# Performance work log

Measured on AMD Instinct MI355X. Metric: run time of the kernel, lower is better.

## Reference

```python
import jax, jax.numpy as jnp
import numpy as np

INPUT_SIZE = 512
OUTPUT_CLASS = 2
BATCH, INST_NUM = 4, 40000


def setup_inputs() -> dict:
    key = jax.random.key(0)
    ks = jax.random.split(key, 8)
    s_in = 1.0 / np.sqrt(INPUT_SIZE)
    s_h = 1.0 / np.sqrt(128)
    return {
        "feats": jax.random.normal(ks[0], (BATCH, INST_NUM, INPUT_SIZE), jnp.float32),
        "c": jax.random.normal(ks[1], (BATCH, INST_NUM, OUTPUT_CLASS), jnp.float32),
        "q_w1": jax.random.uniform(ks[2], (INPUT_SIZE, 128), jnp.float32, -s_in, s_in),
        "q_b1": jax.random.uniform(ks[3], (128,), jnp.float32, -s_in, s_in),
        "q_w2": jax.random.uniform(ks[4], (128, 128), jnp.float32, -s_h, s_h),
        "q_b2": jax.random.uniform(ks[5], (128,), jnp.float32, -s_h, s_h),
        "fcc_w": jax.random.uniform(ks[6], (OUTPUT_CLASS, OUTPUT_CLASS, INPUT_SIZE), jnp.float32, -s_in, s_in),
        "fcc_b": jax.random.uniform(ks[7], (OUTPUT_CLASS,), jnp.float32, -s_in, s_in),
    }


def _q_mlp(x, w1, b1, w2, b2):
    h = jax.nn.relu(x @ w1 + b1)
    return jnp.tanh(h @ w2 + b2)


def reference(feats, c, q_w1, q_b1, q_w2, q_b2, fcc_w, fcc_b):
    batch, inst_num, dim = feats.shape
    V = feats  # passing_v=False -> Identity
    Q = _q_mlp(feats, q_w1, q_b1, q_w2, q_b2)  # [b, n, 128]
    # top instance per class: sort descending, take first -> argmax along instances
    top_idx = jnp.argmax(c, axis=1)  # [b, output_class]
    m_feats = jnp.take_along_axis(feats, top_idx[:, :, None], axis=1)  # [b, oc, dim]
    q_max = _q_mlp(m_feats, q_w1, q_b1, q_w2, q_b2)  # [b, oc, 128]
    # NOTE: original divides by sqrt(Q.shape[1]) == sqrt(inst_num)
    scale = jnp.sqrt(jnp.float32(inst_num))
    A = jnp.einsum('bnk,bok->bno', Q, q_max) / scale  # [b, n, oc]
    A = jax.nn.softmax(A, axis=1)  # softmax over instances
    B = jnp.einsum('bno,bnd->bod', A, V)  # [b, oc, dim]
    # Conv1d(oc, oc, kernel=dim) on B -> full contraction over (in_ch, dim)
    C = jnp.einsum('bid,oid->bo', B, fcc_w) + fcc_b  # [b, oc]
    return C, A, B
```

## Files before the change

### kernel.cpp

```cpp
#include <hip/hip_runtime.h>
#include <hip/hip_bf16.h>

#define NB 4
#define NI 40000
#define DI 512
#define NH 128
#define TM 32
#define NT 1250

typedef __attribute__((ext_vector_type(8))) short bf16x8;
typedef __attribute__((ext_vector_type(4))) float f32x4;

__device__ __forceinline__ ushort f2b(float f) {
    union { float f; unsigned u; } x; x.f = f;
    unsigned r = x.u + 0x7FFFu + ((x.u >> 16) & 1u);
    return (ushort)(r >> 16);
}
__device__ __forceinline__ float b2f(ushort u) {
    union { unsigned u; float f; } x; x.u = ((unsigned)u) << 16;
    return x.f;
}

__global__ void k_wt(const float* __restrict__ w1, const float* __restrict__ w2,
                     ushort* __restrict__ w1t, ushort* __restrict__ w2t) {
    int idx = blockIdx.x * 256 + threadIdx.x;
    if (idx < 65536) {
        int j = idx >> 9, i = idx & 511;
        w1t[idx] = f2b(w1[i * 128 + j]);
    } else if (idx < 81920) {
        int r = idx - 65536;
        int j = r >> 7, k = r & 127;
        w2t[r] = f2b(w2[k * 128 + j]);
    }
}

__global__ void k_am1(const float* __restrict__ c, float* __restrict__ pv, int* __restrict__ pi) {
    int blk = blockIdx.x;
    int bo = blk >> 4, ch = blk & 15;
    int b = bo >> 1, o = bo & 1;
    __shared__ float rv[256];
    __shared__ int   ri[256];
    int tid = threadIdx.x;
    float bv = -3.402823466e38f; int bi = 0x7fffffff;
    for (int n = ch * 2500 + tid; n < (ch + 1) * 2500; n += 256) {
        float v = c[((size_t)b * NI + n) * 2 + o];
        if (v > bv || (v == bv && n < bi)) { bv = v; bi = n; }
    }
    rv[tid] = bv; ri[tid] = bi;
    __syncthreads();
    for (int s = 128; s > 0; s >>= 1) {
        if (tid < s) {
            if (rv[tid + s] > rv[tid] || (rv[tid + s] == rv[tid] && ri[tid + s] < ri[tid])) {
                rv[tid] = rv[tid + s]; ri[tid] = ri[tid + s];
            }
        }
        __syncthreads();
    }
    if (tid == 0) { pv[blk] = rv[0]; pi[blk] = ri[0]; }
}

__global__ void k_am2(const float* __restrict__ pv, const int* __restrict__ pi,
                      int* __restrict__ topidx) {
    int bo = blockIdx.x;
    if (threadIdx.x == 0) {
        float bv = -3.402823466e38f; int bi = 0x7fffffff;
        for (int ch = 0; ch < 16; ++ch) {
            float v = pv[bo * 16 + ch]; int idx = pi[bo * 16 + ch];
            if (v > bv || (v == bv && idx < bi)) { bv = v; bi = idx; }
        }
        topidx[bo] = bi;
    }
}

__global__ void k_qmax(const float* __restrict__ feats, const int* __restrict__ topidx,
                       const float* __restrict__ w1, const float* __restrict__ b1,
                       const float* __restrict__ w2, const float* __restrict__ b2,
                       float* __restrict__ qmax) {
    int bo = blockIdx.x;
    int b = bo >> 1;
    __shared__ float xs[DI];
    __shared__ float hs[NH];
    int tid = threadIdx.x;
    const float* x = feats + ((size_t)b * NI + topidx[bo]) * DI;
    if (tid < DI) xs[tid] = x[tid];
    __syncthreads();
    int j = tid >> 2, part = tid & 3;
    float p = 0.f;
    for (int i = part * 128; i < part * 128 + 128; ++i)
        p += xs[i] * w1[i * NH + j];
    p += __shfl_xor(p, 1); p += __shfl_xor(p, 2);
    if (part == 0) { float h = p + b1[j]; hs[j] = h > 0.f ? h : 0.f; }
    __syncthreads();
    p = 0.f;
    for (int i = part * 32; i < part * 32 + 32; ++i)
        p += hs[i] * w2[i * NH + j];
    p += __shfl_xor(p, 1); p += __shfl_xor(p, 2);
    if (part == 0) qmax[bo * NH + j] = tanhf(p + b2[j]);
}

__global__ __launch_bounds__(256, 3)
void k_main(const float* __restrict__ feats,
            const ushort* __restrict__ w1t, const ushort* __restrict__ w2t,
            const float* __restrict__ b1, const float* __restrict__ b2,
            const float* __restrict__ qmax,
            float* __restrict__ s_ws, float* __restrict__ zp, float* __restrict__ Up) {
    __shared__ ushort x_lds[TM * 512];
    __shared__ ushort h_lds[TM * 128];
    __shared__ float  sp_lds[4][TM][2];
    __shared__ float  e_lds[TM * 2];
    __shared__ float  qm_lds[2 * NH];

    const int tid = threadIdx.x;
    const int b = blockIdx.x / NT;
    const int t = blockIdx.x % NT;
    const int n0 = t * TM;

    qm_lds[tid] = qmax[b * 256 + tid];

    const float4* xg4 = (const float4*)(feats + ((size_t)(b * NI + n0)) * DI);
#pragma unroll
    for (int q = 0; q < 16; ++q) {
        int idx = tid + q * 256;
        int row = idx >> 7;
        int c4  = idx & 127;
        float4 v = xg4[idx];
        ushort4 u;
        u.x = f2b(v.x); u.y = f2b(v.y); u.z = f2b(v.z); u.w = f2b(v.w);
        int byteoff = (c4 * 8) ^ ((row & 7) << 4);
        *(ushort4*)((char*)x_lds + row * 1024 + byteoff) = u;
    }
    __syncthreads();

    const int wn = tid >> 6;
    const int lane = tid & 63;
    const int lr = lane & 15;
    const int lk = (lane >> 4) * 8;
    const int l4 = (lane >> 4) * 4;
    const int xsw = (lr & 7) << 4;

    const char* xrow0 = (const char*)x_lds + lr * 1024;
    const char* xrow1 = (const char*)x_lds + (16 + lr) * 1024;
    const ushort* w1b0 = w1t + (size_t)(wn * 32 + lr) * DI + lk;
    const ushort* w1b1 = w1t + (size_t)(wn * 32 + 16 + lr) * DI + lk;

    f32x4 acc[2][2] = {};
#pragma unroll 4
    for (int ks = 0; ks < 16; ++ks) {
        int kb = (ks * 32 + lk) * 2;
        bf16x8 a0 = *(const bf16x8*)(xrow0 + (kb ^ xsw));
        bf16x8 a1 = *(const bf16x8*)(xrow1 + (kb ^ xsw));
        bf16x8 b0 = *(const bf16x8*)(w1b0 + ks * 32);
        bf16x8 b1v = *(const bf16x8*)(w1b1 + ks * 32);
        acc[0][0] = __builtin_amdgcn_mfma_f32_16x16x32_bf16(a0, b0,  acc[0][0], 0, 0, 0);
        acc[0][1] = __builtin_amdgcn_mfma_f32_16x16x32_bf16(a0, b1v, acc[0][1], 0, 0, 0);
        acc[1][0] = __builtin_amdgcn_mfma_f32_16x16x32_bf16(a1, b0,  acc[1][0], 0, 0, 0);
        acc[1][1] = __builtin_amdgcn_mfma_f32_16x16x32_bf16(a1, b1v, acc[1][1], 0, 0, 0);
    }

#pragma unroll
    for (int m = 0; m < 2; ++m)
#pragma unroll
        for (int n = 0; n < 2; ++n) {
            int col = wn * 32 + n * 16 + lr;
            float bias = b1[col];
#pragma unroll
            for (int r = 0; r < 4; ++r) {
                int row = m * 16 + l4 + r;
                float v = acc[m][n][r] + bias;
                *(ushort*)((char*)h_lds + row * 256 + ((col * 2) ^ ((row & 7) << 4))) =
                    f2b(v > 0.f ? v : 0.f);
            }
        }
    __syncthreads();

    f32x4 acc2[2][2] = {};
#pragma unroll
    for (int ks = 0; ks < 4; ++ks) {
        int kb = (ks * 32 + lk) * 2;
        bf16x8 a0 = *(const bf16x8*)((const char*)h_lds + lr * 256 + (kb ^ xsw));
        bf16x8 a1 = *(const bf16x8*)((const char*)h_lds + (16 + lr) * 256 + (kb ^ xsw));
        bf16x8 b0 = *(const bf16x8*)(w2t + (wn * 32 + lr) * NH + ks * 32 + lk);
        bf16x8 b1v = *(const bf16x8*)(w2t + (wn * 32 + 16 + lr) * NH + ks * 32 + lk);
        acc2[0][0] = __builtin_amdgcn_mfma_f32_16x16x32_bf16(a0, b0,  acc2[0][0], 0, 0, 0);
        acc2[0][1] = __builtin_amdgcn_mfma_f32_16x16x32_bf16(a0, b1v, acc2[0][1], 0, 0, 0);
        acc2[1][0] = __builtin_amdgcn_mfma_f32_16x16x32_bf16(a1, b0,  acc2[1][0], 0, 0, 0);
        acc2[1][1] = __builtin_amdgcn_mfma_f32_16x16x32_bf16(a1, b1v, acc2[1][1], 0, 0, 0);
    }

#pragma unroll
    for (int m = 0; m < 2; ++m)
#pragma unroll
        for (int r = 0; r < 4; ++r) {
            float p0 = 0.f, p1 = 0.f;
#pragma unroll
            for (int n = 0; n < 2; ++n) {
                int col = wn * 32 + n * 16 + lr;
                float q = tanhf(acc2[m][n][r] + b2[col]);
                p0 += q * qm_lds[col];
                p1 += q * qm_lds[NH + col];
            }
            p0 += __shfl_xor(p0, 1); p1 += __shfl_xor(p1, 1);
            p0 += __shfl_xor(p0, 2); p1 += __shfl_xor(p1, 2);
            p0 += __shfl_xor(p0, 4); p1 += __shfl_xor(p1, 4);
            p0 += __shfl_xor(p0, 8); p1 += __shfl_xor(p1, 8);
            if (lr == 0) {
                int row = m * 16 + l4 + r;
                sp_lds[wn][row][0] = p0;
                sp_lds[wn][row][1] = p1;
            }
        }
    __syncthreads();

    if (tid < 64) {
        int row = tid >> 1, o = tid & 1;
        float s = (sp_lds[0][row][o] + sp_lds[1][row][o] +
                   sp_lds[2][row][o] + sp_lds[3][row][o]) * 0.005f;
        s_ws[((size_t)(b * NI + n0 + row)) * 2 + o] = s;
        float e = expf(s);
        e_lds[row * 2 + o] = e;
        float z = e;
        z += __shfl_xor(z, 2);  z += __shfl_xor(z, 4);
        z += __shfl_xor(z, 8);  z += __shfl_xor(z, 16);
        z += __shfl_xor(z, 32);
        if (tid < 2) zp[(b * NT + t) * 2 + tid] = z;
    }
    __syncthreads();

    {
        int bc = tid * 4;
        float u00 = 0.f, u01 = 0.f, u10 = 0.f, u11 = 0.f;
#pragma unroll 8
        for (int n = 0; n < TM; ++n) {
            unsigned v = *(const unsigned*)((const char*)x_lds + n * 1024 + (bc ^ ((n & 7) << 4)));
            float x0 = b2f((ushort)(v & 0xffff));
            float x1 = b2f((ushort)(v >> 16));
            float e0 = e_lds[n * 2], e1 = e_lds[n * 2 + 1];
            u00 += e0 * x0; u01 += e0 * x1;
            u10 += e1 * x0; u11 += e1 * x1;
        }
        size_t base = ((size_t)(b * NT + t) * 2) * DI;
        float2 v0; v0.x = u00; v0.y = u01;
        float2 v1; v1.x = u10; v1.y = u11;
        *(float2*)&Up[base + tid * 2] = v0;
        *(float2*)&Up[base + DI + tid * 2] = v1;
    }
}

__global__ void k_zred(const float* __restrict__ zp, float* __restrict__ Zt) {
    int bo = blockIdx.x; int b = bo >> 1, o = bo & 1;
    __shared__ float red[256];
    int tid = threadIdx.x;
    float z = 0.f;
    for (int t = tid; t < NT; t += 256) z += zp[(b * NT + t) * 2 + o];
    red[tid] = z; __syncthreads();
    for (int s = 128; s > 0; s >>= 1) {
        if (tid < s) red[tid] += red[tid + s];
        __syncthreads();
    }
    if (tid == 0) Zt[bo] = red[0];
}

__global__ void k_A(const float* __restrict__ s_ws, const float* __restrict__ Zt,
                    float* __restrict__ outA) {
    int idx = blockIdx.x * 256 + threadIdx.x;
    int b = idx / (NI * 2);
    int o = idx & 1;
    outA[idx] = expf(s_ws[idx]) / Zt[b * 2 + o];
}

__global__ void k_B1(const float* __restrict__ Up, float* __restrict__ Up2) {
    int blk = blockIdx.x;
    int bo = blk / 25, cch = blk % 25;
    int b = bo >> 1, o = bo & 1;
    int d = threadIdx.x;
    float u = 0.f;
    for (int t = cch * 50; t < cch * 50 + 50; ++t)
        u += Up[(((size_t)(b * NT + t)) * 2 + o) * DI + d];
    Up2[(size_t)blk * DI + d] = u;
}

__global__ void k_B2(const float* __restrict__ Up2, const float* __restrict__ Zt,
                     float* __restrict__ outB) {
    int bo = blockIdx.x; int d = threadIdx.x;
    float u = 0.f;
    for (int cc = 0; cc < 25; ++cc) u += Up2[(size_t)(bo * 25 + cc) * DI + d];
    outB[bo * DI + d] = u / Zt[bo];
}

__global__ void k_C(const float* __restrict__ outB, const float* __restrict__ fcc_w,
                    const float* __restrict__ fcc_b, float* __restrict__ outC) {
    int bo = blockIdx.x; int b = bo >> 1, o = bo & 1;
    __shared__ float red[256];
    int tid = threadIdx.x;
    float acc = 0.f;
    for (int idx = tid; idx < 2 * DI; idx += 256) {
        int i = idx >> 9, d = idx & 511;
        acc += outB[(b * 2 + i) * DI + d] * fcc_w[o * (2 * DI) + i * DI + d];
    }
    red[tid] = acc; __syncthreads();
    for (int s = 128; s > 0; s >>= 1) {
        if (tid < s) red[tid] += red[tid + s];
        __syncthreads();
    }
    if (tid == 0) outC[bo] = red[0] + fcc_b[o];
}

extern "C" void kernel_launch(void* const* d_in, const int* in_sizes, int n_in,
                              void* d_out, int out_size, void* d_ws, size_t ws_size,
                              hipStream_t stream) {
    const float* feats = (const float*)d_in[0];
    const float* c     = (const float*)d_in[1];
    const float* q_w1  = (const float*)d_in[2];
    const float* q_b1  = (const float*)d_in[3];
    const float* q_w2  = (const float*)d_in[4];
    const float* q_b2  = (const float*)d_in[5];
    const float* fcc_w = (const float*)d_in[6];
    const float* fcc_b = (const float*)d_in[7];
    float* out = (float*)d_out;

    char* w = (char*)d_ws;
    ushort* w1t  = (ushort*)(w);
    ushort* w2t  = (ushort*)(w + 131072);
    float* qmaxb = (float*)(w + 163840);
    int*   topi  = (int*)(w + 167936);
    float* Zt    = (float*)(w + 167968);
    float* pv    = (float*)(w + 168000);
    int*   pi    = (int*)(w + 168512);
    float* s_ws  = (float*)(w + 169024);
    float* zp    = (float*)(w + 1449024);
    float* Up2   = (float*)(w + 1489024);
    float* Up    = (float*)(w + 1898624);

    float* outC = out;
    float* outA = out + 8;
    float* outB = out + 8 + NB * NI * 2;

    k_wt<<<320, 256, 0, stream>>>(q_w1, q_w2, w1t, w2t);
    k_am1<<<128, 256, 0, stream>>>(c, pv, pi);
    k_am2<<<8, 64, 0, stream>>>(pv, pi, topi);
    k_qmax<<<8, 512, 0, stream>>>(feats, topi, q_w1, q_b1, q_w2, q_b2, qmaxb);
    k_main<<<NB * NT, 256, 0, stream>>>(feats, w1t, w2t, q_b1, q_b2, qmaxb, s_ws, zp, Up);
    k_zred<<<8, 256, 0, stream>>>(zp, Zt);
    k_A<<<NB * NI * 2 / 256, 256, 0, stream>>>(s_ws, Zt, outA);
    k_B1<<<200, 512, 0, stream>>>(Up, Up2);
    k_B2<<<8, 512, 0, stream>>>(Up2, Zt, outB);
    k_C<<<8, 256, 0, stream>>>(outB, fcc_w, fcc_b, outC);
}
```

Baseline: 204.4 us.

## Make main kernel persistent with double-buffered feature prefetch and register-resident weights

The main kernel becomes persistent: 128 blocks per batch loop over tiles with a stride, prefetching the next tile's features into registers and writing them into a second LDS buffer while the current tile is computed. W2 fragments, biases and qmax values are held in registers, W1 fragments are software-prefetched in groups, and tanh/exp use fast approximations. Per-block partial sums shrink, so the two-stage B reduction collapses into one kernel and the Z reduction uses a single wave. The changes add LDS and register pressure (occupancy bound lowered to 2) and slightly reduce numerical accuracy from the fast tanh/exp.

```diff
diff --git a/kernel.cpp b/kernel.cpp
--- a/kernel.cpp
+++ b/kernel.cpp
@@ -7,6 +7,7 @@
 #define NH 128
 #define TM 32
 #define NT 1250
+#define SUBB 128
 
 typedef __attribute__((ext_vector_type(8))) short bf16x8;
 typedef __attribute__((ext_vector_type(4))) float f32x4;
@@ -19,6 +20,11 @@
 __device__ __forceinline__ float b2f(ushort u) {
     union { unsigned u; float f; } x; x.u = ((unsigned)u) << 16;
     return x.f;
+}
+__device__ __forceinline__ float tanh_fast(float x) {
+    x = fminf(15.f, fmaxf(-15.f, x));
+    float e = __expf(2.f * x);
+    return (e - 1.f) / (e + 1.f);
 }
 
 __global__ void k_wt(const float* __restrict__ w1, const float* __restrict__ w2,
@@ -98,38 +104,51 @@
     if (part == 0) qmax[bo * NH + j] = tanhf(p + b2[j]);
 }
 
-__global__ __launch_bounds__(256, 3)
+#define L1G(C0, C1, N0, N1, G)                                                  \
+  {                                                                             \
+    if ((G) < 3) {                                                              \
+      _Pragma("unroll")                                                         \
+      for (int j = 0; j < 4; ++j) {                                             \
+        N0[j] = *(const bf16x8*)(wb0 + ((G) + 1) * 128 + j * 32);               \
+        N1[j] = *(const bf16x8*)(wb1 + ((G) + 1) * 128 + j * 32);               \
+      }                                                                         \
+    }                                                                           \
+    _Pragma("unroll")                                                           \
+    for (int j = 0; j < 4; ++j) {                                               \
+      int kb = (((G) * 4 + j) * 32 + lk) * 2;                                   \
+      bf16x8 a0 = *(const bf16x8*)(xrow0 + (kb ^ xsw));                         \
+      bf16x8 a1 = *(const bf16x8*)(xrow1 + (kb ^ xsw));                         \
+      acc00 = __builtin_amdgcn_mfma_f32_16x16x32_bf16(a0, C0[j], acc00, 0, 0, 0);\
+      acc01 = __builtin_amdgcn_mfma_f32_16x16x32_bf16(a0, C1[j], acc01, 0, 0, 0);\
+      acc10 = __builtin_amdgcn_mfma_f32_16x16x32_bf16(a1, C0[j], acc10, 0, 0, 0);\
+      acc11 = __builtin_amdgcn_mfma_f32_16x16x32_bf16(a1, C1[j], acc11, 0, 0, 0);\
+    }                                                                           \
+  }
+
+#define EPI1(ACC, M, N, BIAS)                                                   \
+  _Pragma("unroll")                                                             \
+  for (int r = 0; r < 4; ++r) {                                                 \
+    int row = (M) * 16 + l4 + r;                                                \
+    float v = ACC[r] + (BIAS);                                                  \
+    *(ushort*)((char*)h_lds + row * 256 +                                       \
+               (((wn * 32 + (N) * 16 + lr) * 2) ^ ((row & 7) << 4))) =          \
+        f2b(v > 0.f ? v : 0.f);                                                 \
+  }
+
+__global__ __launch_bounds__(256, 2)
 void k_main(const float* __restrict__ feats,
             const ushort* __restrict__ w1t, const ushort* __restrict__ w2t,
             const float* __restrict__ b1, const float* __restrict__ b2,
             const float* __restrict__ qmax,
             float* __restrict__ s_ws, float* __restrict__ zp, float* __restrict__ Up) {
-    __shared__ ushort x_lds[TM * 512];
+    __shared__ ushort x_lds[2 * TM * 512];
     __shared__ ushort h_lds[TM * 128];
     __shared__ float  sp_lds[4][TM][2];
     __shared__ float  e_lds[TM * 2];
-    __shared__ float  qm_lds[2 * NH];
 
     const int tid = threadIdx.x;
-    const int b = blockIdx.x / NT;
-    const int t = blockIdx.x % NT;
-    const int n0 = t * TM;
-
-    qm_lds[tid] = qmax[b * 256 + tid];
-
-    const float4* xg4 = (const float4*)(feats + ((size_t)(b * NI + n0)) * DI);
-#pragma unroll
-    for (int q = 0; q < 16; ++q) {
-        int idx = tid + q * 256;
-        int row = idx >> 7;
-        int c4  = idx & 127;
-        float4 v = xg4[idx];
-        ushort4 u;
-        u.x = f2b(v.x); u.y = f2b(v.y); u.z = f2b(v.z); u.w = f2b(v.w);
-        int byteoff = (c4 * 8) ^ ((row & 7) << 4);
-        *(ushort4*)((char*)x_lds + row * 1024 + byteoff) = u;
-    }
-    __syncthreads();
+    const int sub = blockIdx.x & (SUBB - 1);
+    const int b   = blockIdx.x >> 7;
 
     const int wn = tid >> 6;
     const int lane = tid & 63;
@@ -138,126 +157,174 @@
     const int l4 = (lane >> 4) * 4;
     const int xsw = (lr & 7) << 4;
 
-    const char* xrow0 = (const char*)x_lds + lr * 1024;
-    const char* xrow1 = (const char*)x_lds + (16 + lr) * 1024;
-    const ushort* w1b0 = w1t + (size_t)(wn * 32 + lr) * DI + lk;
-    const ushort* w1b1 = w1t + (size_t)(wn * 32 + 16 + lr) * DI + lk;
-
-    f32x4 acc[2][2] = {};
-#pragma unroll 4
-    for (int ks = 0; ks < 16; ++ks) {
-        int kb = (ks * 32 + lk) * 2;
-        bf16x8 a0 = *(const bf16x8*)(xrow0 + (kb ^ xsw));
-        bf16x8 a1 = *(const bf16x8*)(xrow1 + (kb ^ xsw));
-        bf16x8 b0 = *(const bf16x8*)(w1b0 + ks * 32);
-        bf16x8 b1v = *(const bf16x8*)(w1b1 + ks * 32);
-        acc[0][0] = __builtin_amdgcn_mfma_f32_16x16x32_bf16(a0, b0,  acc[0][0], 0, 0, 0);
-        acc[0][1] = __builtin_amdgcn_mfma_f32_16x16x32_bf16(a0, b1v, acc[0][1], 0, 0, 0);
-        acc[1][0] = __builtin_amdgcn_mfma_f32_16x16x32_bf16(a1, b0,  acc[1][0], 0, 0, 0);
-        acc[1][1] = __builtin_amdgcn_mfma_f32_16x16x32_bf16(a1, b1v, acc[1][1], 0, 0, 0);
-    }
-
-#pragma unroll
-    for (int m = 0; m < 2; ++m)
-#pragma unroll
-        for (int n = 0; n < 2; ++n) {
-            int col = wn * 32 + n * 16 + lr;
-            float bias = b1[col];
+    const int col0 = wn * 32 + lr;
+    const int col1 = col0 + 16;
+    const float rb1_0 = b1[col0], rb1_1 = b1[col1];
+    const float rb2_0 = b2[col0], rb2_1 = b2[col1];
+    const float qm00 = qmax[b * 256 + col0];
+    const float qm01 = qmax[b * 256 + col1];
+    const float qm10 = qmax[b * 256 + NH + col0];
+    const float qm11 = qmax[b * 256 + NH + col1];
+
+    bf16x8 W2f0[4], W2f1[4];
+#pragma unroll
+    for (int ks = 0; ks < 4; ++ks) {
+        W2f0[ks] = *(const bf16x8*)&w2t[(size_t)col0 * NH + ks * 32 + lk];
+        W2f1[ks] = *(const bf16x8*)&w2t[(size_t)col1 * NH + ks * 32 + lk];
+    }
+
+    const ushort* wb0 = w1t + (size_t)(wn * 32 + lr) * DI + lk;
+    const ushort* wb1 = wb0 + (size_t)16 * DI;
+
+    float u00 = 0.f, u01 = 0.f, u10 = 0.f, u11 = 0.f;
+    float zacc = 0.f;
+
+    float4 pf[16];
+
+    {
+        const float4* xg4 = (const float4*)(feats + ((size_t)b * NI + sub * TM) * DI);
+#pragma unroll
+        for (int q = 0; q < 16; ++q) pf[q] = xg4[tid + q * 256];
+#pragma unroll
+        for (int q = 0; q < 16; ++q) {
+            int idx = tid + q * 256;
+            int row = idx >> 7, c4 = idx & 127;
+            unsigned lo, hi;
+            asm("v_cvt_pk_bf16_f32 %0, %1, %2" : "=v"(lo) : "v"(pf[q].x), "v"(pf[q].y));
+            asm("v_cvt_pk_bf16_f32 %0, %1, %2" : "=v"(hi) : "v"(pf[q].z), "v"(pf[q].w));
+            uint2 u; u.x = lo; u.y = hi;
+            *(uint2*)((char*)x_lds + row * 1024 + ((c4 * 8) ^ ((row & 7) << 4))) = u;
+        }
+    }
+    __syncthreads();
+
+    int cur = 0;
+    for (int t = sub; t < NT; t += SUBB) {
+        const int nxt = cur ^ 1;
+        const bool more = (t + SUBB < NT);
+
+        if (more) {
+            const float4* xg4 = (const float4*)(feats + ((size_t)b * NI + (t + SUBB) * TM) * DI);
+#pragma unroll
+            for (int q = 0; q < 16; ++q) pf[q] = xg4[tid + q * 256];
+        }
+
+        const char* xrow0 = (const char*)x_lds + cur * 32768 + lr * 1024;
+        const char* xrow1 = (const char*)x_lds + cur * 32768 + (16 + lr) * 1024;
+
+        f32x4 acc00 = {}, acc01 = {}, acc10 = {}, acc11 = {};
+        bf16x8 BA0[4], BA1[4], BB0[4], BB1[4];
+#pragma unroll
+        for (int j = 0; j < 4; ++j) {
+            BA0[j] = *(const bf16x8*)(wb0 + j * 32);
+            BA1[j] = *(const bf16x8*)(wb1 + j * 32);
+        }
+        L1G(BA0, BA1, BB0, BB1, 0)
+        L1G(BB0, BB1, BA0, BA1, 1)
+        L1G(BA0, BA1, BB0, BB1, 2)
+        L1G(BB0, BB1, BA0, BA1, 3)
+
+        EPI1(acc00, 0, 0, rb1_0)
+        EPI1(acc01, 0, 1, rb1_1)
+        EPI1(acc10, 1, 0, rb1_0)
+        EPI1(acc11, 1, 1, rb1_1)
+        __syncthreads();
+
+        f32x4 c200 = {}, c201 = {}, c210 = {}, c211 = {};
+#pragma unroll
+        for (int ks = 0; ks < 4; ++ks) {
+            int kb = (ks * 32 + lk) * 2;
+            bf16x8 a0 = *(const bf16x8*)((const char*)h_lds + lr * 256 + (kb ^ xsw));
+            bf16x8 a1 = *(const bf16x8*)((const char*)h_lds + (16 + lr) * 256 + (kb ^ xsw));
+            c200 = __builtin_amdgcn_mfma_f32_16x16x32_bf16(a0, W2f0[ks], c200, 0, 0, 0);
+            c201 = __builtin_amdgcn_mfma_f32_16x16x32_bf16(a0, W2f1[ks], c201, 0, 0, 0);
+            c210 = __builtin_amdgcn_mfma_f32_16x16x32_bf16(a1, W2f0[ks], c210, 0, 0, 0);
+            c211 = __builtin_amdgcn_mfma_f32_16x16x32_bf16(a1, W2f1[ks], c211, 0, 0, 0);
+        }
+
+#pragma unroll
+        for (int m = 0; m < 2; ++m)
 #pragma unroll
             for (int r = 0; r < 4; ++r) {
-                int row = m * 16 + l4 + r;
-                float v = acc[m][n][r] + bias;
-                *(ushort*)((char*)h_lds + row * 256 + ((col * 2) ^ ((row & 7) << 4))) =
-                    f2b(v > 0.f ? v : 0.f);
+                float q0 = tanh_fast((m ? c210[r] : c200[r]) + rb2_0);
+                float q1 = tanh_fast((m ? c211[r] : c201[r]) + rb2_1);
+                float p0 = q0 * qm00 + q1 * qm01;
+                float p1 = q0 * qm10 + q1 * qm11;
+                p0 += __shfl_xor(p0, 1); p1 += __shfl_xor(p1, 1);
+                p0 += __shfl_xor(p0, 2); p1 += __shfl_xor(p1, 2);
+                p0 += __shfl_xor(p0, 4); p1 += __shfl_xor(p1, 4);
+                p0 += __shfl_xor(p0, 8); p1 += __shfl_xor(p1, 8);
+                if (lr == 0) {
+                    int row = m * 16 + l4 + r;
+                    sp_lds[wn][row][0] = p0;
+                    sp_lds[wn][row][1] = p1;
+                }
             }
-        }
-    __syncthreads();
-
-    f32x4 acc2[2][2] = {};
-#pragma unroll
-    for (int ks = 0; ks < 4; ++ks) {
-        int kb = (ks * 32 + lk) * 2;
-        bf16x8 a0 = *(const bf16x8*)((const char*)h_lds + lr * 256 + (kb ^ xsw));
-        bf16x8 a1 = *(const bf16x8*)((const char*)h_lds + (16 + lr) * 256 + (kb ^ xsw));
-        bf16x8 b0 = *(const bf16x8*)(w2t + (wn * 32 + lr) * NH + ks * 32 + lk);
-        bf16x8 b1v = *(const bf16x8*)(w2t + (wn * 32 + 16 + lr) * NH + ks * 32 + lk);
-        acc2[0][0] = __builtin_amdgcn_mfma_f32_16x16x32_bf16(a0, b0,  acc2[0][0], 0, 0, 0);
-        acc2[0][1] = __builtin_amdgcn_mfma_f32_16x16x32_bf16(a0, b1v, acc2[0][1], 0, 0, 0);
-        acc2[1][0] = __builtin_amdgcn_mfma_f32_16x16x32_bf16(a1, b0,  acc2[1][0], 0, 0, 0);
-        acc2[1][1] = __builtin_amdgcn_mfma_f32_16x16x32_bf16(a1, b1v, acc2[1][1], 0, 0, 0);
-    }
-
-#pragma unroll
-    for (int m = 0; m < 2; ++m)
-#pragma unroll
-        for (int r = 0; r < 4; ++r) {
-            float p0 = 0.f, p1 = 0.f;
-#pragma unroll
-            for (int n = 0; n < 2; ++n) {
-                int col = wn * 32 + n * 16 + lr;
-                float q = tanhf(acc2[m][n][r] + b2[col]);
-                p0 += q * qm_lds[col];
-                p1 += q * qm_lds[NH + col];
+        __syncthreads();
+
+        if (tid < 64) {
+            int row = tid >> 1, o = tid & 1;
+            float s = (sp_lds[0][row][o] + sp_lds[1][row][o] +
+                       sp_lds[2][row][o] + sp_lds[3][row][o]) * 0.005f;
+            s_ws[((size_t)(b * NI + t * TM + row)) * 2 + o] = s;
+            float e = __expf(s);
+            e_lds[row * 2 + o] = e;
+            float z = e;
+            z += __shfl_xor(z, 2);  z += __shfl_xor(z, 4);
+            z += __shfl_xor(z, 8);  z += __shfl_xor(z, 16);
+            z += __shfl_xor(z, 32);
+            if (tid < 2) zacc += z;
+        }
+
+        if (more) {
+#pragma unroll
+            for (int q = 0; q < 16; ++q) {
+                int idx = tid + q * 256;
+                int row = idx >> 7, c4 = idx & 127;
+                unsigned lo, hi;
+                asm("v_cvt_pk_bf16_f32 %0, %1, %2" : "=v"(lo) : "v"(pf[q].x), "v"(pf[q].y));
+                asm("v_cvt_pk_bf16_f32 %0, %1, %2" : "=v"(hi) : "v"(pf[q].z), "v"(pf[q].w));
+                uint2 u; u.x = lo; u.y = hi;
+                *(uint2*)((char*)x_lds + nxt * 32768 + row * 1024 + ((c4 * 8) ^ ((row & 7) << 4))) = u;
             }
-            p0 += __shfl_xor(p0, 1); p1 += __shfl_xor(p1, 1);
-            p0 += __shfl_xor(p0, 2); p1 += __shfl_xor(p1, 2);
-            p0 += __shfl_xor(p0, 4); p1 += __shfl_xor(p1, 4);
-            p0 += __shfl_xor(p0, 8); p1 += __shfl_xor(p1, 8);
-            if (lr == 0) {
-                int row = m * 16 + l4 + r;
-                sp_lds[wn][row][0] = p0;
-                sp_lds[wn][row][1] = p1;
+        }
+        __syncthreads();
+
+        {
+            int bc = tid * 4;
+#pragma unroll 8
+            for (int n = 0; n < TM; ++n) {
+                unsigned v = *(const unsigned*)((const char*)x_lds + cur * 32768 +
+                                                n * 1024 + (bc ^ ((n & 7) << 4)));
+                float x0 = b2f((ushort)(v & 0xffff));
+                float x1 = b2f((ushort)(v >> 16));
+                float e0 = e_lds[n * 2], e1 = e_lds[n * 2 + 1];
+                u00 += e0 * x0; u01 += e0 * x1;
+                u10 += e1 * x0; u11 += e1 * x1;
             }
         }
-    __syncthreads();
-
-    if (tid < 64) {
-        int row = tid >> 1, o = tid & 1;
-        float s = (sp_lds[0][row][o] + sp_lds[1][row][o] +
-                   sp_lds[2][row][o] + sp_lds[3][row][o]) * 0.005f;
-        s_ws[((size_t)(b * NI + n0 + row)) * 2 + o] = s;
-        float e = expf(s);
-        e_lds[row * 2 + o] = e;
-        float z = e;
-        z += __shfl_xor(z, 2);  z += __shfl_xor(z, 4);
-        z += __shfl_xor(z, 8);  z += __shfl_xor(z, 16);
-        z += __shfl_xor(z, 32);
-        if (tid < 2) zp[(b * NT + t) * 2 + tid] = z;
-    }
-    __syncthreads();
+        __syncthreads();
+        cur = nxt;
+    }
 
     {
-        int bc = tid * 4;
-        float u00 = 0.f, u01 = 0.f, u10 = 0.f, u11 = 0.f;
-#pragma unroll 8
-        for (int n = 0; n < TM; ++n) {
-            unsigned v = *(const unsigned*)((const char*)x_lds + n * 1024 + (bc ^ ((n & 7) << 4)));
-            float x0 = b2f((ushort)(v & 0xffff));
-            float x1 = b2f((ushort)(v >> 16));
-            float e0 = e_lds[n * 2], e1 = e_lds[n * 2 + 1];
-            u00 += e0 * x0; u01 += e0 * x1;
-            u10 += e1 * x0; u11 += e1 * x1;
-        }
-        size_t base = ((size_t)(b * NT + t) * 2) * DI;
+        size_t base = ((size_t)(b * SUBB + sub) * 2) * DI;
         float2 v0; v0.x = u00; v0.y = u01;
         float2 v1; v1.x = u10; v1.y = u11;
         *(float2*)&Up[base + tid * 2] = v0;
         *(float2*)&Up[base + DI + tid * 2] = v1;
+        if (tid < 2) zp[(b * SUBB + sub) * 2 + tid] = zacc;
     }
 }
 
 __global__ void k_zred(const float* __restrict__ zp, float* __restrict__ Zt) {
     int bo = blockIdx.x; int b = bo >> 1, o = bo & 1;
-    __shared__ float red[256];
     int tid = threadIdx.x;
-    float z = 0.f;
-    for (int t = tid; t < NT; t += 256) z += zp[(b * NT + t) * 2 + o];
-    red[tid] = z; __syncthreads();
-    for (int s = 128; s > 0; s >>= 1) {
-        if (tid < s) red[tid] += red[tid + s];
-        __syncthreads();
-    }
-    if (tid == 0) Zt[bo] = red[0];
+    float z = zp[((b * SUBB + tid) * 2) + o] + zp[((b * SUBB + tid + 64) * 2) + o];
+    z += __shfl_xor(z, 1);  z += __shfl_xor(z, 2);
+    z += __shfl_xor(z, 4);  z += __shfl_xor(z, 8);
+    z += __shfl_xor(z, 16); z += __shfl_xor(z, 32);
+    if (tid == 0) Zt[bo] = z;
 }
 
 __global__ void k_A(const float* __restrict__ s_ws, const float* __restrict__ Zt,
@@ -265,25 +332,16 @@
     int idx = blockIdx.x * 256 + threadIdx.x;
     int b = idx / (NI * 2);
     int o = idx & 1;
-    outA[idx] = expf(s_ws[idx]) / Zt[b * 2 + o];
-}
-
-__global__ void k_B1(const float* __restrict__ Up, float* __restrict__ Up2) {
-    int blk = blockIdx.x;
-    int bo = blk / 25, cch = blk % 25;
+    outA[idx] = __expf(s_ws[idx]) / Zt[b * 2 + o];
+}
+
+__global__ void k_B(const float* __restrict__ Up, const float* __restrict__ Zt,
+                    float* __restrict__ outB) {
+    int bo = blockIdx.x; int d = threadIdx.x;
     int b = bo >> 1, o = bo & 1;
-    int d = threadIdx.x;
     float u = 0.f;
-    for (int t = cch * 50; t < cch * 50 + 50; ++t)
-        u += Up[(((size_t)(b * NT + t)) * 2 + o) * DI + d];
-    Up2[(size_t)blk * DI + d] = u;
-}
-
-__global__ void k_B2(const float* __restrict__ Up2, const float* __restrict__ Zt,
-                     float* __restrict__ outB) {
-    int bo = blockIdx.x; int d = threadIdx.x;
-    float u = 0.f;
-    for (int cc = 0; cc < 25; ++cc) u += Up2[(size_t)(bo * 25 + cc) * DI + d];
+    for (int s2 = 0; s2 < SUBB; ++s2)
+        u += Up[(((size_t)(b * SUBB + s2)) * 2 + o) * DI + d];
     outB[bo * DI + d] = u / Zt[bo];
 }
 
@@ -328,8 +386,7 @@
     int*   pi    = (int*)(w + 168512);
     float* s_ws  = (float*)(w + 169024);
     float* zp    = (float*)(w + 1449024);
-    float* Up2   = (float*)(w + 1489024);
-    float* Up    = (float*)(w + 1898624);
+    float* Up    = (float*)(w + 1453120);
 
     float* outC = out;
     float* outA = out + 8;
@@ -339,10 +396,9 @@
     k_am1<<<128, 256, 0, stream>>>(c, pv, pi);
     k_am2<<<8, 64, 0, stream>>>(pv, pi, topi);
     k_qmax<<<8, 512, 0, stream>>>(feats, topi, q_w1, q_b1, q_w2, q_b2, qmaxb);
-    k_main<<<NB * NT, 256, 0, stream>>>(feats, w1t, w2t, q_b1, q_b2, qmaxb, s_ws, zp, Up);
-    k_zred<<<8, 256, 0, stream>>>(zp, Zt);
+    k_main<<<NB * SUBB, 256, 0, stream>>>(feats, w1t, w2t, q_b1, q_b2, qmaxb, s_ws, zp, Up);
+    k_zred<<<8, 64, 0, stream>>>(zp, Zt);
     k_A<<<NB * NI * 2 / 256, 256, 0, stream>>>(s_ws, Zt, outA);
-    k_B1<<<200, 512, 0, stream>>>(Up, Up2);
-    k_B2<<<8, 512, 0, stream>>>(Up2, Zt, outB);
+    k_B<<<8, 512, 0, stream>>>(Up, Zt, outB);
     k_C<<<8, 256, 0, stream>>>(outB, fcc_w, fcc_b, outC);
 }
```

Result: slower. 363.6 us (+77.9%).
